# Performance work log

Measured on AMD Instinct MI355X. Metric: run time of the kernel, lower is better.

## Reference

```python
import jax, jax.numpy as jnp
import numpy as np

BS, CAMS, NQ, EMBED = 1, 6, 6400, 256
HEADS, LEVELS, POINTS, DEPTH = 8, 4, 8, 4
DH = EMBED // HEADS
SHAPES = np.array([[64, 176], [32, 88], [16, 44], [8, 22]], dtype=np.int64)  # (H, W) per level
FLEN = int((SHAPES[:, 0] * SHAPES[:, 1]).sum())  # 14960


def setup_inputs() -> dict:
    key = jax.random.key(0)
    ks = jax.random.split(key, 12)
    s = 0.02
    lsi = np.concatenate([[0], np.cumsum(SHAPES[:, 0] * SHAPES[:, 1])[:-1]]).astype(np.int64)
    return {
        'query': jax.random.normal(ks[0], (BS, NQ, EMBED), jnp.float32),
        'key': jax.random.normal(ks[1], (BS, FLEN, CAMS, EMBED), jnp.float32),
        'value': jax.random.normal(ks[2], (BS, FLEN, CAMS, EMBED), jnp.float32),
        'query_pos': jax.random.normal(ks[3], (BS, NQ, EMBED), jnp.float32),
        'reference_points_cam': jax.random.uniform(ks[4], (CAMS, BS, NQ, DEPTH, 2), jnp.float32),
        'bev_mask': jax.random.bernoulli(ks[5], 0.1, (CAMS, BS, NQ, DEPTH)),
        'spatial_shapes': jnp.asarray(SHAPES),
        'level_start_index': jnp.asarray(lsi),
        'Wv': jax.random.normal(ks[6], (EMBED, EMBED), jnp.float32) * s,
        'bv': jnp.zeros((EMBED,), jnp.float32),
        'Wso': jax.random.normal(ks[7], (EMBED, HEADS * LEVELS * POINTS * 2), jnp.float32) * s,
        'bso': jax.random.normal(ks[8], (HEADS * LEVELS * POINTS * 2,), jnp.float32) * s,
        'Waw': jax.random.normal(ks[9], (EMBED, HEADS * LEVELS * POINTS), jnp.float32) * s,
        'baw': jnp.zeros((HEADS * LEVELS * POINTS,), jnp.float32),
        'Wout': jax.random.normal(ks[10], (EMBED, EMBED), jnp.float32) * s,
        'bout': jnp.zeros((EMBED,), jnp.float32),
    }


def _bilinear_gather(v, xi, yi, Wl, Hl):
    # v: (B, Hl*Wl, H, Dh); xi, yi: (B, Nq, H, P) integer-valued floats.
    # grid_sample(padding_mode='zeros'): out-of-range corners contribute 0.
    valid = (xi >= 0) & (xi < Wl) & (yi >= 0) & (yi < Hl)
    idx = (jnp.clip(yi, 0, Hl - 1) * Wl + jnp.clip(xi, 0, Wl - 1)).astype(jnp.int32)
    B, Nq, Hh, P = idx.shape
    idx2 = idx.transpose(0, 1, 3, 2).reshape(B, Nq * P, Hh)[..., None]
    g = jnp.take_along_axis(v, idx2, axis=1)  # (B, Nq*P, Hh, Dh)
    g = g.reshape(B, Nq, P, Hh, -1).transpose(0, 1, 3, 2, 4)  # (B, Nq, Hh, P, Dh)
    return jnp.where(valid[..., None], g, 0.0)


def _msda(v, loc, aw):
    # Multi-scale deformable attn: v (B, Len, H, Dh); loc in [0,1] (B, Nq, H, L, P, 2); aw (B, Nq, H, L, P).
    out = 0.0
    start = 0
    for l in range(LEVELS):
        Hl, Wl = int(SHAPES[l, 0]), int(SHAPES[l, 1])
        vl = v[:, start:start + Hl * Wl]
        start += Hl * Wl
        # align_corners=False pixel coords
        x = loc[:, :, :, l, :, 0] * Wl - 0.5
        y = loc[:, :, :, l, :, 1] * Hl - 0.5
        x0 = jnp.floor(x)
        y0 = jnp.floor(y)
        wx1 = x - x0
        wy1 = y - y0
        s = (_bilinear_gather(vl, x0, y0, Wl, Hl) * ((1 - wx1) * (1 - wy1))[..., None]
             + _bilinear_gather(vl, x0 + 1, y0, Wl, Hl) * (wx1 * (1 - wy1))[..., None]
             + _bilinear_gather(vl, x0, y0 + 1, Wl, Hl) * ((1 - wx1) * wy1)[..., None]
             + _bilinear_gather(vl, x0 + 1, y0 + 1, Wl, Hl) * (wx1 * wy1)[..., None])
        out = out + jnp.einsum('bqhpd,bqhp->bqhd', s, aw[:, :, :, l])
    B, Nq = out.shape[0], out.shape[1]
    return out.reshape(B, Nq, -1)


def reference(query, key, value, query_pos, reference_points_cam, bev_mask,
              spatial_shapes, level_start_index, Wv, bv, Wso, bso, Waw, baw, Wout, bout):
    bs, nq, C = query.shape
    cams = bev_mask.shape[0]
    inp_residual = query  # residual is taken BEFORE query_pos is added
    q = query + query_pos
    # per-camera query visibility from batch-0 mask (as in the torch loop over bev_mask)
    mask_q = jnp.any(bev_mask[:, 0], axis=-1)  # (cams, nq)
    # instead of gather-rebatch to max_len, run attention for all queries and mask the scatter-add
    q_cam = jnp.broadcast_to(q[:, None], (bs, cams, nq, C)).reshape(bs * cams, nq, C)
    ref = jnp.transpose(reference_points_cam, (1, 0, 2, 3, 4)).reshape(bs * cams, nq, DEPTH, 2)
    v = jnp.transpose(value, (2, 0, 1, 3)).reshape(bs * cams, -1, C)
    # MSDeformableAttention3D (BEVFormer): value_proj, offsets, softmax weights, bilinear sampling
    v = (v @ Wv + bv).reshape(bs * cams, -1, HEADS, DH)
    off = (q_cam @ Wso + bso).reshape(bs * cams, nq, HEADS, LEVELS, POINTS, 2)
    norm = jnp.stack([spatial_shapes[:, 1], spatial_shapes[:, 0]], -1).astype(off.dtype)  # (L, 2) = (W, H)
    off = off / norm[None, None, None, :, None, :]
    aw = jax.nn.softmax((q_cam @ Waw + baw).reshape(bs * cams, nq, HEADS, LEVELS * POINTS), axis=-1)
    aw = aw.reshape(bs * cams, nq, HEADS, LEVELS, POINTS)
    pa = POINTS // DEPTH  # xy points per Z anchor
    loc = ref[:, :, None, None, None, :, :] + off.reshape(bs * cams, nq, HEADS, LEVELS, pa, DEPTH, 2)
    loc = loc.reshape(bs * cams, nq, HEADS, LEVELS, POINTS, 2)
    out = _msda(v, loc, aw).reshape(bs, cams, nq, C)
    # scatter-add back: slots[b, q] += sum_cam visible(cam, q) * out[b, cam, q]
    slots = jnp.sum(out * mask_q[None, :, :, None].astype(out.dtype), axis=1)
    count = jnp.any(bev_mask, axis=-1).transpose(1, 2, 0).sum(-1).astype(slots.dtype)  # (bs, nq)
    count = jnp.maximum(count, 1.0)
    slots = slots / count[..., None]
    slots = slots @ Wout + bout
    return slots + inp_residual  # dropout in eval mode = identity
```

## Files before the change

### kernel.cpp

```cpp
#include <hip/hip_runtime.h>
#include <hip/hip_bf16.h>

#define CAMS   6
#define NQ     6400
#define EMBED  256
#define HEADS  8
#define LEVELS 4
#define POINTS 8
#define DEPTH  4
#define DH     32
#define FLEN   14960
#define MV     (FLEN * CAMS)
#define NCHUNK 2805
#define NQCHUNK 200

__constant__ int c_LW[4] = {176, 88, 44, 22};
__constant__ int c_LH[4] = {64, 32, 16, 8};
__constant__ int c_LS[4] = {0, 11264, 14080, 14784};

typedef __bf16 bf16x8 __attribute__((ext_vector_type(8)));
typedef float  f32x4  __attribute__((ext_vector_type(4)));

__device__ __forceinline__ ushort f2bf(float x) {
    __hip_bfloat16 h = __float2bfloat16(x);
    return *(ushort*)&h;
}
__device__ __forceinline__ float bflo(unsigned u) { return __uint_as_float(u << 16); }
__device__ __forceinline__ float bfhi(unsigned u) { return __uint_as_float(u & 0xffff0000u); }

__device__ __forceinline__ bf16x8 pack8(float4 a, float4 b) {
    union { ushort u[8]; bf16x8 v; } r;
    r.u[0] = f2bf(a.x); r.u[1] = f2bf(a.y); r.u[2] = f2bf(a.z); r.u[3] = f2bf(a.w);
    r.u[4] = f2bf(b.x); r.u[5] = f2bf(b.y); r.u[6] = f2bf(b.z); r.u[7] = f2bf(b.w);
    return r.v;
}

#define LSTRIDE 40

__device__ __forceinline__ void gemm_body_out(ushort* sA, ushort* sB,
                                              const float* __restrict__ A,
                                              const float* __restrict__ W, int ldw,
                                              const float* __restrict__ bias,
                                              const float* __restrict__ resid,
                                              float* __restrict__ Cout, int ldc, int M,
                                              int bx, int by) {
    const int t = threadIdx.x;
    const int wave = t >> 6;
    const int lane = t & 63;
    const int wm = wave & 1, wn = wave >> 1;
    const int lane15 = lane & 15;
    const int laneq = lane >> 4;
    const int row0 = bx * 128;
    const int col0 = by * 128;

    f32x4 acc[4][4] = {};

    const int a_m = t >> 3;
    const int a_k = (t & 7) * 4;
    const int b_n = t & 127;
    const int b_k = (t >> 7) * 4;

    float4 aR[4], wR[4];

    #pragma unroll
    for (int p = 0; p < 4; ++p) {
        int gm = row0 + a_m + p * 32;
        if (gm >= M) gm = M - 1;
        aR[p] = *(const float4*)(A + (size_t)gm * 256 + a_k);
    }
    #pragma unroll
    for (int p = 0; p < 4; ++p) {
        const int k = b_k + p * 8;
        const float* wp = W + (size_t)k * ldw + col0 + b_n;
        wR[p] = make_float4(wp[0], wp[ldw], wp[2 * ldw], wp[3 * ldw]);
    }

    for (int k0 = 0; k0 < 256; k0 += 32) {
        #pragma unroll
        for (int p = 0; p < 4; ++p) {
            const int m = a_m + p * 32;
            const float4 a4 = aR[p];
            *(ushort4*)(&sA[m * LSTRIDE + a_k]) =
                make_ushort4(f2bf(a4.x), f2bf(a4.y), f2bf(a4.z), f2bf(a4.w));
        }
        #pragma unroll
        for (int p = 0; p < 4; ++p) {
            const int k = b_k + p * 8;
            *(ushort4*)(&sB[b_n * LSTRIDE + k]) =
                make_ushort4(f2bf(wR[p].x), f2bf(wR[p].y), f2bf(wR[p].z), f2bf(wR[p].w));
        }
        __syncthreads();

        if (k0 + 32 < 256) {
            #pragma unroll
            for (int p = 0; p < 4; ++p) {
                int gm = row0 + a_m + p * 32;
                if (gm >= M) gm = M - 1;
                aR[p] = *(const float4*)(A + (size_t)gm * 256 + k0 + 32 + a_k);
            }
            #pragma unroll
            for (int p = 0; p < 4; ++p) {
                const int k = b_k + p * 8;
                const float* wp = W + (size_t)(k0 + 32 + k) * ldw + col0 + b_n;
                wR[p] = make_float4(wp[0], wp[ldw], wp[2 * ldw], wp[3 * ldw]);
            }
        }

        bf16x8 af[4], bfr[4];
        #pragma unroll
        for (int i = 0; i < 4; ++i) {
            const int m = wm * 64 + i * 16 + lane15;
            af[i] = *(const bf16x8*)(&sA[m * LSTRIDE + laneq * 8]);
            const int n = wn * 64 + i * 16 + lane15;
            bfr[i] = *(const bf16x8*)(&sB[n * LSTRIDE + laneq * 8]);
        }
        #pragma unroll
        for (int i = 0; i < 4; ++i)
            #pragma unroll
            for (int j = 0; j < 4; ++j)
                acc[i][j] = __builtin_amdgcn_mfma_f32_16x16x32_bf16(af[i], bfr[j], acc[i][j], 0, 0, 0);
        __syncthreads();
    }

    #pragma unroll
    for (int j = 0; j < 4; ++j) {
        const int col = col0 + wn * 64 + j * 16 + lane15;
        const float bcol = bias[col];
        #pragma unroll
        for (int i = 0; i < 4; ++i) {
            #pragma unroll
            for (int r = 0; r < 4; ++r) {
                const int row = row0 + wm * 64 + i * 16 + laneq * 4 + r;
                if (row < M) {
                    float v = acc[i][j][r] + bcol + resid[(size_t)row * 256 + col];
                    Cout[(size_t)row * ldc + col] = v;
                }
            }
        }
    }
}

__device__ __forceinline__ void add4(float4& a, float4 b) {
    a.x += b.x; a.y += b.y; a.z += b.z; a.w += b.w;
}

template <int QMODE>
__device__ __forceinline__ void wstat_body(ushort* sW,
                                           const float* __restrict__ A,
                                           const float* __restrict__ A2,
                                           const float* __restrict__ W, int ldw, int c0,
                                           const float* __restrict__ bias,
                                           void* __restrict__ out, int ldc,
                                           int nchunk, int blk, int nblk) {
    const int t = threadIdx.x;

    {
        const int n = t;
        const int xr = (n & 7) << 3;
        #pragma unroll 8
        for (int r = 0; r < 64; ++r) {
            const int k4 = r * 4;
            const float w0 = W[(size_t)(k4 + 0) * ldw + c0 + n];
            const float w1 = W[(size_t)(k4 + 1) * ldw + c0 + n];
            const float w2 = W[(size_t)(k4 + 2) * ldw + c0 + n];
            const float w3 = W[(size_t)(k4 + 3) * ldw + c0 + n];
            *(ushort4*)(&sW[n * 256 + (k4 ^ xr)]) =
                make_ushort4(f2bf(w0), f2bf(w1), f2bf(w2), f2bf(w3));
        }
    }
    __syncthreads();

    const int wave = t >> 6, lane = t & 63;
    const int lane15 = lane & 15, laneq = lane >> 4;

    float bcol[16];
    #pragma unroll
    for (int nt = 0; nt < 16; ++nt) bcol[nt] = bias[c0 + nt * 16 + lane15];

    for (int c = blk * 4 + wave; c < nchunk; c += nblk * 4) {
        const int rowbase = c * 32;
        const float* ap0 = A + (size_t)(rowbase + lane15) * 256 + laneq * 8;
        const float* ap1 = ap0 + 16 * 256;

        float4 a[2][8][2];
        #pragma unroll
        for (int s = 0; s < 8; ++s) {
            a[0][s][0] = *(const float4*)(ap0 + s * 32);
            a[0][s][1] = *(const float4*)(ap0 + s * 32 + 4);
            a[1][s][0] = *(const float4*)(ap1 + s * 32);
            a[1][s][1] = *(const float4*)(ap1 + s * 32 + 4);
        }
        if (QMODE == 1) {
            const float* bp0 = A2 + (size_t)(rowbase + lane15) * 256 + laneq * 8;
            const float* bp1 = bp0 + 16 * 256;
            #pragma unroll
            for (int s = 0; s < 8; ++s) {
                add4(a[0][s][0], *(const float4*)(bp0 + s * 32));
                add4(a[0][s][1], *(const float4*)(bp0 + s * 32 + 4));
                add4(a[1][s][0], *(const float4*)(bp1 + s * 32));
                add4(a[1][s][1], *(const float4*)(bp1 + s * 32 + 4));
            }
        }

        f32x4 acc[2][16] = {};
        #pragma unroll
        for (int s = 0; s < 8; ++s) {
            const bf16x8 fa0 = pack8(a[0][s][0], a[0][s][1]);
            const bf16x8 fa1 = pack8(a[1][s][0], a[1][s][1]);
            const int kb = laneq * 8 + s * 32;
            #pragma unroll
            for (int nt = 0; nt < 16; ++nt) {
                const int n = nt * 16 + lane15;
                const bf16x8 fb = *(const bf16x8*)(&sW[n * 256 + (kb ^ ((n & 7) << 3))]);
                acc[0][nt] = __builtin_amdgcn_mfma_f32_16x16x32_bf16(fa0, fb, acc[0][nt], 0, 0, 0);
                acc[1][nt] = __builtin_amdgcn_mfma_f32_16x16x32_bf16(fa1, fb, acc[1][nt], 0, 0, 0);
            }
        }

        #pragma unroll
        for (int rt = 0; rt < 2; ++rt) {
            #pragma unroll
            for (int r = 0; r < 4; ++r) {
                const int row = rowbase + rt * 16 + laneq * 4 + r;
                if (QMODE == 0) {
                    const unsigned pix = ((unsigned)row * 43691u) >> 18;
                    const unsigned cam = (unsigned)row - pix * 6u;
                    const unsigned base = (cam * 8u * FLEN + pix) * 32u;
                    #pragma unroll
                    for (int nt = 0; nt < 16; ++nt) {
                        const unsigned idx = base + (unsigned)(nt >> 1) * (FLEN * 32u)
                                           + (unsigned)((nt & 1) * 16 + lane15);
                        ((ushort*)out)[idx] = f2bf(acc[rt][nt][r] + bcol[nt]);
                    }
                } else {
                    float* op = (float*)out + (size_t)row * ldc + c0 + lane15;
                    #pragma unroll
                    for (int nt = 0; nt < 16; ++nt)
                        op[nt * 16] = acc[rt][nt][r] + bcol[nt];
                }
            }
        }
    }
}

__launch_bounds__(256, 1)
__global__ void fused_pre_gemm(const float* __restrict__ value,
                               const float* __restrict__ query,
                               const float* __restrict__ query_pos,
                               const float* __restrict__ Wv,  const float* __restrict__ bv,
                               const float* __restrict__ Wso, const float* __restrict__ bso,
                               const float* __restrict__ Waw, const float* __restrict__ baw,
                               const void* __restrict__ bm,
                               ushort* __restrict__ v_ws,
                               float* __restrict__ off_ws,
                               float* __restrict__ aw_ws,
                               int* __restrict__ flag) {
    __shared__ ushort sW[256 * 256];
    const int bid = blockIdx.x;
    if (bid < 211) {
        wstat_body<0>(sW, value, nullptr, Wv, 256, 0, bv, v_ws, 0, NCHUNK, bid, 211);
    } else if (bid < 226) {
        wstat_body<1>(sW, query, query_pos, Wso, 512, 0,   bso, off_ws, 512, NQCHUNK, bid - 211, 15);
    } else if (bid < 241) {
        wstat_body<1>(sW, query, query_pos, Wso, 512, 256, bso, off_ws, 512, NQCHUNK, bid - 226, 15);
    } else if (bid < 256) {
        wstat_body<1>(sW, query, query_pos, Waw, 256, 0,   baw, aw_ws, 256, NQCHUNK, bid - 241, 15);
    } else {
        const int t = threadIdx.x;
        const uint4* p4 = (const uint4*)bm;
        unsigned acc = 0;
        for (int i = t; i < (CAMS * NQ * DEPTH) / 16; i += 256) {
            const uint4 w = p4[i];
            acc |= w.x | w.y | w.z | w.w;
        }
        #pragma unroll
        for (int off = 32; off >= 1; off >>= 1) acc |= __shfl_xor(acc, off);
        unsigned* sred = (unsigned*)sW;
        if ((t & 63) == 0) sred[t >> 6] = acc;
        __syncthreads();
        if (t == 0) {
            const unsigned a = sred[0] | sred[1] | sred[2] | sred[3];
            flag[0] = (a & 0xFFFFFF00u) ? 1 : 0;
        }
    }
}

__launch_bounds__(256)
__global__ void gemm_out_kernel(const float* __restrict__ slots,
                                const float* __restrict__ Wout,
                                const float* __restrict__ bout,
                                const float* __restrict__ query,
                                float* __restrict__ out) {
    __shared__ ushort sA[128 * LSTRIDE];
    __shared__ ushort sB[128 * LSTRIDE];
    const int bid = blockIdx.x;
    gemm_body_out(sA, sB, slots, Wout, 256, bout, query, out, 256, NQ, bid >> 1, bid & 1);
}

#define STAGE(ADDR, WGT, UU, CAM) do {                                          \
    const int cam_ = (CAM);                                                     \
    const float4 r01_ = *(const float4*)(rp + (size_t)cam_ * (NQ * 8) + q * 8); \
    const float4 r23_ = *(const float4*)(rp + (size_t)cam_ * (NQ * 8) + q * 8 + 4); \
    const float rx_[4] = {r01_.x, r01_.z, r23_.x, r23_.z};                      \
    const float ry_[4] = {r01_.y, r01_.w, r23_.y, r23_.w};                      \
    const int camhF_ = (cam_ * 8 + h) * FLEN + St;                              \
    _Pragma("unroll")                                                           \
    for (int j = 0; j < 4; ++j) {                                               \
        const float x = fmaf(rx_[j], fWl, offx[j]) - 0.5f;                      \
        const float y = fmaf(ry_[j], fHl, offy[j]) - 0.5f;                      \
        const float x0f = floorf(x), y0f = floorf(y);                           \
        const int x0 = (int)x0f, y0 = (int)y0f;                                 \
        const float fx = x - x0f, fy = y - y0f;                                 \
        const float wx0 = 1.f - fx, wy0 = 1.f - fy;                             \
        _Pragma("unroll")                                                       \
        for (int cc = 0; cc < 4; ++cc) {                                        \
            const int cx = x0 + (cc & 1);                                       \
            const int cy = y0 + (cc >> 1);                                      \
            const bool valid = ((unsigned)cx < (unsigned)Wl) & ((unsigned)cy < (unsigned)Hl); \
            const int pixo = valid ? (cy * Wl + cx) : 0;                        \
            ADDR[j * 4 + cc] = ((camhF_ + pixo) << 5) + ch8;                    \
            WGT[j * 4 + cc] = valid                                             \
                ? (((cc & 1) ? fx : wx0) * ((cc >> 1) ? fy : wy0) * awv[j])     \
                : 0.f;                                                          \
        }                                                                       \
    }                                                                           \
    _Pragma("unroll")                                                           \
    for (int i = 0; i < 16; ++i) UU[i] = *(const uint4*)(v + ADDR[i]);          \
} while (0)

#define CONSUME(UU, WGT) do {                                                   \
    _Pragma("unroll")                                                           \
    for (int i = 0; i < 16; ++i) {                                              \
        const uint4 u = UU[i];                                                  \
        const float w = WGT[i];                                                 \
        accv[0] = fmaf(w, bflo(u.x), accv[0]);                                  \
        accv[1] = fmaf(w, bfhi(u.x), accv[1]);                                  \
        accv[2] = fmaf(w, bflo(u.y), accv[2]);                                  \
        accv[3] = fmaf(w, bfhi(u.y), accv[3]);                                  \
        accv[4] = fmaf(w, bflo(u.z), accv[4]);                                  \
        accv[5] = fmaf(w, bfhi(u.z), accv[5]);                                  \
        accv[6] = fmaf(w, bflo(u.w), accv[6]);                                  \
        accv[7] = fmaf(w, bfhi(u.w), accv[7]);                                  \
    }                                                                           \
} while (0)

__launch_bounds__(256)
__global__ void sample_kernel(const ushort* __restrict__ v,
                              const float* __restrict__ off_ws,
                              const float* __restrict__ aw_logit,
                              const float* __restrict__ rp,
                              const void* __restrict__ bm,
                              const int* __restrict__ flag,
                              float* __restrict__ slots) {
    const int q = blockIdx.x;
    const int t = threadIdx.x;
    const int h = t >> 5;
    const int e8 = (t >> 2) & 7;
    const int ch8 = (t & 3) * 8;
    const int l = e8 >> 1;
    const int ebase = h * 32 + e8 * 4;

    const int Wl = c_LW[l], Hl = c_LH[l], St = c_LS[l];
    const float fWl = (float)Wl, fHl = (float)Hl;

    const int fmt = *flag;
    int am = 0, cnt = 0;
    if (fmt == 1) {
        #pragma unroll
        for (int cam = 0; cam < CAMS; ++cam) {
            const unsigned w = ((const unsigned*)bm)[cam * NQ + q];
            const int a = (w != 0u);
            am |= a << cam;
            cnt += a;
        }
    } else {
        #pragma unroll
        for (int cam = 0; cam < CAMS; ++cam) {
            const int4 w = ((const int4*)bm)[cam * NQ + q];
            const int a = ((w.x | w.y | w.z | w.w) != 0);
            am |= a << cam;
            cnt += a;
        }
    }
    const float invq = 1.0f / (float)(cnt > 0 ? cnt : 1);

    const float4 lg = *(const float4*)(aw_logit + (size_t)q * 256 + ebase);
    float mx = fmaxf(fmaxf(lg.x, lg.y), fmaxf(lg.z, lg.w));
    mx = fmaxf(mx, __shfl_xor(mx, 4));
    mx = fmaxf(mx, __shfl_xor(mx, 8));
    mx = fmaxf(mx, __shfl_xor(mx, 16));
    const float e0 = expf(lg.x - mx), e1 = expf(lg.y - mx);
    const float e2 = expf(lg.z - mx), e3 = expf(lg.w - mx);
    float s = e0 + e1 + e2 + e3;
    s += __shfl_xor(s, 4);
    s += __shfl_xor(s, 8);
    s += __shfl_xor(s, 16);
    const float sc = invq / s;
    const float awv[4] = {e0 * sc, e1 * sc, e2 * sc, e3 * sc};

    const float* ofp = off_ws + (size_t)q * 512 + ebase * 2;
    const float4 o01 = *(const float4*)(ofp);
    const float4 o23 = *(const float4*)(ofp + 4);
    const float offx[4] = {o01.x, o01.z, o23.x, o23.z};
    const float offy[4] = {o01.y, o01.w, o23.y, o23.w};

    float accv[8] = {};

    int   addrA[16], addrB[16];
    float wgtA[16], wgtB[16];
    uint4 uA[16], uB[16];

    int m = am;
    int camA = -1;
    if (m) { camA = __ffs(m) - 1; m &= m - 1; STAGE(addrA, wgtA, uA, camA); }

    #pragma unroll
    for (int it = 0; it < 3; ++it) {
        if (camA < 0) break;
        int camB = -1;
        if (m) { camB = __ffs(m) - 1; m &= m - 1; STAGE(addrB, wgtB, uB, camB); }
        CONSUME(uA, wgtA);
        camA = -1;
        if (camB < 0) break;
        if (m) { camA = __ffs(m) - 1; m &= m - 1; STAGE(addrA, wgtA, uA, camA); }
        CONSUME(uB, wgtB);
    }

    #pragma unroll
    for (int i = 0; i < 8; ++i) {
        accv[i] += __shfl_xor(accv[i], 4);
        accv[i] += __shfl_xor(accv[i], 8);
        accv[i] += __shfl_xor(accv[i], 16);
    }
    slots[(size_t)q * 256 + h * 32 + ch8 + e8] = accv[e8];
}

extern "C" void kernel_launch(void* const* d_in, const int* in_sizes, int n_in,
                              void* d_out, int out_size, void* d_ws, size_t ws_size,
                              hipStream_t stream) {
    const float* query     = (const float*)d_in[0];
    const float* value     = (const float*)d_in[2];
    const float* query_pos = (const float*)d_in[3];
    const float* refpts    = (const float*)d_in[4];
    const void*  bev_mask  = d_in[5];
    const float* Wv   = (const float*)d_in[8];
    const float* bv   = (const float*)d_in[9];
    const float* Wso  = (const float*)d_in[10];
    const float* bso  = (const float*)d_in[11];
    const float* Waw  = (const float*)d_in[12];
    const float* baw  = (const float*)d_in[13];
    const float* Wout = (const float*)d_in[14];
    const float* bout = (const float*)d_in[15];
    float* out = (float*)d_out;

    ushort* v_ws  = (ushort*)d_ws;
    float* off_ws = (float*)(v_ws + (size_t)MV * 256);
    float* aw_ws  = off_ws + (size_t)NQ * 512;
    float* slots  = aw_ws + (size_t)NQ * 256;
    int*   flag   = (int*)(slots + (size_t)NQ * 256);

    hipLaunchKernelGGL(fused_pre_gemm, dim3(257), dim3(256), 0, stream,
                       value, query, query_pos, Wv, bv, Wso, bso, Waw, baw,
                       bev_mask, v_ws, off_ws, aw_ws, flag);

    hipLaunchKernelGGL(sample_kernel, dim3(NQ), dim3(256), 0, stream,
                       v_ws, off_ws, aw_ws, refpts, bev_mask, flag, slots);

    hipLaunchKernelGGL(gemm_out_kernel, dim3(100), dim3(256), 0, stream,
                       slots, Wout, bout, query, out);
}
```

Before: 370.8 us.

## Split sampling across a camera grid dimension with atomic accumulation into slots

The sample kernel now launches one block per (query, camera) pair instead of looping over visible cameras inside one block. Blocks for invisible cameras exit early, and the visible ones atomically add their partial result into a slots buffer that is zeroed by a memset beforehand. The aim is more parallelism and latency hiding than the serial double-buffered camera loop gave. The cost is six times as many blocks (most of which exit immediately), a redundant mask and softmax computation per camera, atomics, and an extra memset.

```diff
diff --git a/kernel.cpp b/kernel.cpp
--- a/kernel.cpp
+++ b/kernel.cpp
@@ -297,53 +297,6 @@
     gemm_body_out(sA, sB, slots, Wout, 256, bout, query, out, 256, NQ, bid >> 1, bid & 1);
 }
 
-#define STAGE(ADDR, WGT, UU, CAM) do {                                          \
-    const int cam_ = (CAM);                                                     \
-    const float4 r01_ = *(const float4*)(rp + (size_t)cam_ * (NQ * 8) + q * 8); \
-    const float4 r23_ = *(const float4*)(rp + (size_t)cam_ * (NQ * 8) + q * 8 + 4); \
-    const float rx_[4] = {r01_.x, r01_.z, r23_.x, r23_.z};                      \
-    const float ry_[4] = {r01_.y, r01_.w, r23_.y, r23_.w};                      \
-    const int camhF_ = (cam_ * 8 + h) * FLEN + St;                              \
-    _Pragma("unroll")                                                           \
-    for (int j = 0; j < 4; ++j) {                                               \
-        const float x = fmaf(rx_[j], fWl, offx[j]) - 0.5f;                      \
-        const float y = fmaf(ry_[j], fHl, offy[j]) - 0.5f;                      \
-        const float x0f = floorf(x), y0f = floorf(y);                           \
-        const int x0 = (int)x0f, y0 = (int)y0f;                                 \
-        const float fx = x - x0f, fy = y - y0f;                                 \
-        const float wx0 = 1.f - fx, wy0 = 1.f - fy;                             \
-        _Pragma("unroll")                                                       \
-        for (int cc = 0; cc < 4; ++cc) {                                        \
-            const int cx = x0 + (cc & 1);                                       \
-            const int cy = y0 + (cc >> 1);                                      \
-            const bool valid = ((unsigned)cx < (unsigned)Wl) & ((unsigned)cy < (unsigned)Hl); \
-            const int pixo = valid ? (cy * Wl + cx) : 0;                        \
-            ADDR[j * 4 + cc] = ((camhF_ + pixo) << 5) + ch8;                    \
-            WGT[j * 4 + cc] = valid                                             \
-                ? (((cc & 1) ? fx : wx0) * ((cc >> 1) ? fy : wy0) * awv[j])     \
-                : 0.f;                                                          \
-        }                                                                       \
-    }                                                                           \
-    _Pragma("unroll")                                                           \
-    for (int i = 0; i < 16; ++i) UU[i] = *(const uint4*)(v + ADDR[i]);          \
-} while (0)
-
-#define CONSUME(UU, WGT) do {                                                   \
-    _Pragma("unroll")                                                           \
-    for (int i = 0; i < 16; ++i) {                                              \
-        const uint4 u = UU[i];                                                  \
-        const float w = WGT[i];                                                 \
-        accv[0] = fmaf(w, bflo(u.x), accv[0]);                                  \
-        accv[1] = fmaf(w, bfhi(u.x), accv[1]);                                  \
-        accv[2] = fmaf(w, bflo(u.y), accv[2]);                                  \
-        accv[3] = fmaf(w, bfhi(u.y), accv[3]);                                  \
-        accv[4] = fmaf(w, bflo(u.z), accv[4]);                                  \
-        accv[5] = fmaf(w, bfhi(u.z), accv[5]);                                  \
-        accv[6] = fmaf(w, bflo(u.w), accv[6]);                                  \
-        accv[7] = fmaf(w, bfhi(u.w), accv[7]);                                  \
-    }                                                                           \
-} while (0)
-
 __launch_bounds__(256)
 __global__ void sample_kernel(const ushort* __restrict__ v,
                               const float* __restrict__ off_ws,
@@ -352,7 +305,8 @@
                               const void* __restrict__ bm,
                               const int* __restrict__ flag,
                               float* __restrict__ slots) {
-    const int q = blockIdx.x;
+    const int q   = blockIdx.x;
+    const int cam = blockIdx.y;
     const int t = threadIdx.x;
     const int h = t >> 5;
     const int e8 = (t >> 2) & 7;
@@ -360,29 +314,32 @@
     const int l = e8 >> 1;
     const int ebase = h * 32 + e8 * 4;
 
-    const int Wl = c_LW[l], Hl = c_LH[l], St = c_LS[l];
-    const float fWl = (float)Wl, fHl = (float)Hl;
+    unsigned wa[CAMS];
+    #pragma unroll
+    for (int c = 0; c < CAMS; ++c) wa[c] = ((const unsigned*)bm)[c * NQ + q];
+    const float4 r01 = *(const float4*)(rp + (size_t)cam * (NQ * 8) + q * 8);
+    const float4 r23 = *(const float4*)(rp + (size_t)cam * (NQ * 8) + q * 8 + 4);
 
     const int fmt = *flag;
     int am = 0, cnt = 0;
     if (fmt == 1) {
         #pragma unroll
-        for (int cam = 0; cam < CAMS; ++cam) {
-            const unsigned w = ((const unsigned*)bm)[cam * NQ + q];
-            const int a = (w != 0u);
-            am |= a << cam;
+        for (int c = 0; c < CAMS; ++c) {
+            const int a = (wa[c] != 0u);
+            am |= a << c;
             cnt += a;
         }
     } else {
         #pragma unroll
-        for (int cam = 0; cam < CAMS; ++cam) {
-            const int4 w = ((const int4*)bm)[cam * NQ + q];
+        for (int c = 0; c < CAMS; ++c) {
+            const int4 w = ((const int4*)bm)[c * NQ + q];
             const int a = ((w.x | w.y | w.z | w.w) != 0);
-            am |= a << cam;
+            am |= a << c;
             cnt += a;
         }
     }
-    const float invq = 1.0f / (float)(cnt > 0 ? cnt : 1);
+    if (!((am >> cam) & 1)) return;
+    const float invq = 1.0f / (float)cnt;
 
     const float4 lg = *(const float4*)(aw_logit + (size_t)q * 256 + ebase);
     float mx = fmaxf(fmaxf(lg.x, lg.y), fmaxf(lg.z, lg.w));
@@ -404,26 +361,49 @@
     const float offx[4] = {o01.x, o01.z, o23.x, o23.z};
     const float offy[4] = {o01.y, o01.w, o23.y, o23.w};
 
+    const int Wl = c_LW[l], Hl = c_LH[l], St = c_LS[l];
+    const float fWl = (float)Wl, fHl = (float)Hl;
+
+    const float rx[4] = {r01.x, r01.z, r23.x, r23.z};
+    const float ry[4] = {r01.y, r01.w, r23.y, r23.w};
+    const int camhF = (cam * 8 + h) * FLEN + St;
+
+    int   addr[16];
+    float wgt[16];
+    #pragma unroll
+    for (int j = 0; j < 4; ++j) {
+        const float x = fmaf(rx[j], fWl, offx[j]) - 0.5f;
+        const float y = fmaf(ry[j], fHl, offy[j]) - 0.5f;
+        const float x0f = floorf(x), y0f = floorf(y);
+        const int x0 = (int)x0f, y0 = (int)y0f;
+        const float fx = x - x0f, fy = y - y0f;
+        const float wx0 = 1.f - fx, wy0 = 1.f - fy;
+        #pragma unroll
+        for (int c = 0; c < 4; ++c) {
+            const int cx = x0 + (c & 1);
+            const int cy = y0 + (c >> 1);
+            const bool valid = ((unsigned)cx < (unsigned)Wl) & ((unsigned)cy < (unsigned)Hl);
+            const int pixo = valid ? (cy * Wl + cx) : 0;
+            addr[j * 4 + c] = ((camhF + pixo) << 5) + ch8;
+            wgt[j * 4 + c] = valid
+                ? (((c & 1) ? fx : wx0) * ((c >> 1) ? fy : wy0) * awv[j])
+                : 0.f;
+        }
+    }
+
     float accv[8] = {};
-
-    int   addrA[16], addrB[16];
-    float wgtA[16], wgtB[16];
-    uint4 uA[16], uB[16];
-
-    int m = am;
-    int camA = -1;
-    if (m) { camA = __ffs(m) - 1; m &= m - 1; STAGE(addrA, wgtA, uA, camA); }
-
-    #pragma unroll
-    for (int it = 0; it < 3; ++it) {
-        if (camA < 0) break;
-        int camB = -1;
-        if (m) { camB = __ffs(m) - 1; m &= m - 1; STAGE(addrB, wgtB, uB, camB); }
-        CONSUME(uA, wgtA);
-        camA = -1;
-        if (camB < 0) break;
-        if (m) { camA = __ffs(m) - 1; m &= m - 1; STAGE(addrA, wgtA, uA, camA); }
-        CONSUME(uB, wgtB);
+    #pragma unroll
+    for (int i = 0; i < 16; ++i) {
+        const uint4 u = *(const uint4*)(v + addr[i]);
+        const float w = wgt[i];
+        accv[0] = fmaf(w, bflo(u.x), accv[0]);
+        accv[1] = fmaf(w, bfhi(u.x), accv[1]);
+        accv[2] = fmaf(w, bflo(u.y), accv[2]);
+        accv[3] = fmaf(w, bfhi(u.y), accv[3]);
+        accv[4] = fmaf(w, bflo(u.z), accv[4]);
+        accv[5] = fmaf(w, bfhi(u.z), accv[5]);
+        accv[6] = fmaf(w, bflo(u.w), accv[6]);
+        accv[7] = fmaf(w, bfhi(u.w), accv[7]);
     }
 
     #pragma unroll
@@ -432,7 +412,7 @@
         accv[i] += __shfl_xor(accv[i], 8);
         accv[i] += __shfl_xor(accv[i], 16);
     }
-    slots[(size_t)q * 256 + h * 32 + ch8 + e8] = accv[e8];
+    atomicAdd(&slots[(size_t)q * 256 + h * 32 + ch8 + e8], accv[e8]);
 }
 
 extern "C" void kernel_launch(void* const* d_in, const int* in_sizes, int n_in,
@@ -459,11 +439,13 @@
     float* slots  = aw_ws + (size_t)NQ * 256;
     int*   flag   = (int*)(slots + (size_t)NQ * 256);
 
+    hipMemsetAsync(slots, 0, (size_t)NQ * 256 * sizeof(float), stream);
+
     hipLaunchKernelGGL(fused_pre_gemm, dim3(257), dim3(256), 0, stream,
                        value, query, query_pos, Wv, bv, Wso, bso, Waw, baw,
                        bev_mask, v_ws, off_ws, aw_ws, flag);
 
-    hipLaunchKernelGGL(sample_kernel, dim3(NQ), dim3(256), 0, stream,
+    hipLaunchKernelGGL(sample_kernel, dim3(NQ, CAMS), dim3(256), 0, stream,
                        v_ws, off_ws, aw_ws, refpts, bev_mask, flag, slots);
 
     hipLaunchKernelGGL(gemm_out_kernel, dim3(100), dim3(256), 0, stream,
```

Measured after the change: 370.2 us. No clear change (-0.2%).
